# Optimization experiments

Measured on AMD Instinct MI355X. Metric: run time of the kernel, lower is better.

Reference implementation:

```python
import jax, jax.numpy as jnp
import numpy as np

B, D, E, H, TOP_K = 8192, 1024, 16, 1024, 8
LOSS_COEF = 0.01
NOISE_EPS = 0.01
INV_SQRT2 = 0.7071067811865476


def _normal_cdf(z):
    return 0.5 * (1.0 + jax.lax.erf(z * INV_SQRT2))


def _cv_squared(v):
    v = v.astype(jnp.float32)
    return jnp.var(v, ddof=1) / (jnp.mean(v) ** 2 + 1e-10)


def setup_inputs() -> dict:
    key = jax.random.key(0)
    k1, k2, k3, k4, k5, k6 = jax.random.split(key, 6)
    return {
        "x": jax.random.normal(k1, (B, D), dtype=jnp.float32),
        "w_gate": jax.random.normal(k2, (D, E), dtype=jnp.float32) * 0.02,
        "w_noise": jax.random.normal(k3, (D, E), dtype=jnp.float32) * 0.02,
        "expert_w": jax.random.normal(k4, (E, D, H), dtype=jnp.float32) * (1.0 / np.sqrt(D)),
        "expert_b": jax.random.normal(k5, (E, H), dtype=jnp.float32) * 0.01,
        "noise": jax.random.normal(k6, (B, E), dtype=jnp.float32),
    }


def reference(x, w_gate, w_noise, expert_w, expert_b, noise):
    # ---- noisy top-k gating (training=True) ----
    clean_logits = x @ w_gate                                   # [B, E]
    raw_noise_stddev = x @ w_noise                              # [B, E]
    noise_stddev = jax.nn.softplus(raw_noise_stddev) + NOISE_EPS
    noisy_logits = clean_logits + noise * noise_stddev          # [B, E]
    probs = jax.nn.softmax(noisy_logits, axis=1)                # [B, E]

    m = min(TOP_K + 1, E)
    top_logits, top_indices = jax.lax.top_k(probs, m)           # [B, m]
    top_k_logits = top_logits[:, :TOP_K]
    top_k_indices = top_indices[:, :TOP_K]
    top_k_gates = top_k_logits / (jnp.sum(top_k_logits, axis=1, keepdims=True) + 1e-6)

    rows = jnp.arange(B)[:, None]
    gates = jnp.zeros_like(probs).at[rows, top_k_indices].set(top_k_gates)  # [B, E]

    # ---- prob-in-top-k load (top_k < num_experts, training) ----
    # faithful to source: thresholds come from softmaxed top values,
    # compared against pre-softmax noisy/clean logits (as in original code)
    threshold_if_in = top_logits[:, TOP_K][:, None]             # [B, 1]
    threshold_if_out = top_logits[:, TOP_K - 1][:, None]        # [B, 1]
    is_in = noisy_logits > threshold_if_in
    prob_if_in = _normal_cdf((clean_logits - threshold_if_in) / noise_stddev)
    prob_if_out = _normal_cdf((clean_logits - threshold_if_out) / noise_stddev)
    load = jnp.where(is_in, prob_if_in, prob_if_out).sum(axis=0)  # [E]

    importance = gates.sum(axis=0)                              # [E]
    loss = LOSS_COEF * (_cv_squared(importance) + _cv_squared(load))

    # ---- experts: per-expert linear, gate-weighted sum over experts ----
    # y[b,h] = sum_e gates[b,e] * (x[b,:] @ W[e] + b[e])[h]
    y = jnp.einsum('bd,edh,be->bh', x, expert_w, gates) + gates @ expert_b
    return y, loss
```

## Files before the change

### kernel.cpp

```cpp
#include <hip/hip_runtime.h>
#include <cstdint>

#define B_SZ 8192
#define D_SZ 1024
#define E_SZ 16
#define H_SZ 1024
#define MAXTILES 544

using short8 = __attribute__((ext_vector_type(8))) short;
using f32x4  = __attribute__((ext_vector_type(4))) float;

__device__ __forceinline__ unsigned short f2bf(float f) {
  union { float f; unsigned int u; } v; v.f = f;
  unsigned int u = v.u;
  return (unsigned short)((u + 0x7fffu + ((u >> 16) & 1u)) >> 16);
}
__device__ __forceinline__ float bf2f(unsigned short h) {
  union { unsigned int u; float f; } v; v.u = ((unsigned int)h) << 16; return v.f;
}

__device__ __forceinline__ void async_ld16(void* lds, const void* g) {
  __builtin_amdgcn_global_load_lds(
      reinterpret_cast<const unsigned int __attribute__((address_space(1)))*>(
          reinterpret_cast<uintptr_t>(g)),
      reinterpret_cast<unsigned int __attribute__((address_space(3)))*>(
          reinterpret_cast<uintptr_t>(lds)),
      16, 0, 0);
}

__global__ __launch_bounds__(256) void prep(
    const float* __restrict__ x, const float* __restrict__ wg,
    const float* __restrict__ wn, const float* __restrict__ ew,
    unsigned short* __restrict__ xb, unsigned short* __restrict__ wtb,
    float* __restrict__ cl, float* __restrict__ rn, float* __restrict__ stats) {
  __shared__ __align__(16) float psm[2 * 32 * 132];
  const int bx = blockIdx.x;
  const int tid = threadIdx.x;

  if (bx < 256) {
    float* sx  = psm;
    float* swT = psm + 32 * 132;
    const int lane = tid & 63;
    const int wave = tid >> 6;
    const int row  = lane & 31;
    const int half = lane >> 5;
    const int rowbase = bx * 32;
    float acc[8] = {0.f, 0.f, 0.f, 0.f, 0.f, 0.f, 0.f, 0.f};

    const int srow = tid >> 3;
    const int sd   = (tid & 7) * 16;
    const int wd   = tid >> 1;
    const int wc   = (tid & 1) * 16;
    const float* wsrc = (wc == 0) ? wg : wn;

    for (int ch = 0; ch < 8; ++ch) {
      __syncthreads();
      #pragma unroll
      for (int k = 0; k < 4; ++k) {
        const float4 v = *(const float4*)(
            x + (size_t)(rowbase + srow) * D_SZ + ch * 128 + sd + k * 4);
        *(float4*)&sx[srow * 132 + sd + k * 4] = v;
      }
      {
        const float* wp = wsrc + (size_t)(ch * 128 + wd) * 16;
        float wv[16];
        #pragma unroll
        for (int k = 0; k < 4; ++k)
          *(float4*)&wv[k * 4] = *(const float4*)(wp + k * 4);
        #pragma unroll
        for (int j = 0; j < 16; ++j) swT[(wc + j) * 132 + wd] = wv[j];
      }
      __syncthreads();
      #pragma unroll 4
      for (int dg = 0; dg < 16; ++dg) {
        const int d = half * 64 + dg * 4;
        const f32x4 xv = *(const f32x4*)&sx[row * 132 + d];
        #pragma unroll
        for (int c = 0; c < 8; ++c) {
          const f32x4 wv = *(const f32x4*)&swT[(wave * 8 + c) * 132 + d];
          acc[c] = fmaf(xv[0], wv[0], acc[c]);
          acc[c] = fmaf(xv[1], wv[1], acc[c]);
          acc[c] = fmaf(xv[2], wv[2], acc[c]);
          acc[c] = fmaf(xv[3], wv[3], acc[c]);
        }
      }
    }
    #pragma unroll
    for (int c = 0; c < 8; ++c) acc[c] += __shfl_down(acc[c], 32);
    if (lane < 32) {
      const int cg = wave * 8;
      float* dst = (cg < 16) ? (cl + (size_t)(rowbase + row) * 16 + cg)
                             : (rn + (size_t)(rowbase + row) * 16 + (cg - 16));
      *(float4*)dst = *(const float4*)&acc[0];
      *(float4*)(dst + 4) = *(const float4*)&acc[4];
    }
  } else if (bx < 4352) {
    const int b = bx - 256;
    const size_t i = (size_t)b * 256 + tid;
    const float4 v0 = ((const float4*)x)[2 * i];
    const float4 v1 = ((const float4*)x)[2 * i + 1];
    unsigned short r[8] = {f2bf(v0.x), f2bf(v0.y), f2bf(v0.z), f2bf(v0.w),
                           f2bf(v1.x), f2bf(v1.y), f2bf(v1.z), f2bf(v1.w)};
    ((short8*)xb)[i] = *(const short8*)r;
    if (b == 0 && tid < 48) stats[tid] = 0.0f;
  } else {
    float (*t)[65] = (float(*)[65])psm;
    const int b = bx - 4352;
    const int e  = b >> 8;
    const int d0 = ((b >> 4) & 15) * 64;
    const int h0 = (b & 15) * 64;
    const float* We = ew + (size_t)e * D_SZ * H_SZ;
    unsigned short* Wte = wtb + (size_t)e * D_SZ * H_SZ;
    #pragma unroll
    for (int i = 0; i < 4; ++i) {
      const int idx = i * 256 + tid;
      const int r = idx >> 4, co = (idx & 15) * 4;
      *(float4*)&t[r][co] =
          *(const float4*)(We + (size_t)(d0 + r) * H_SZ + h0 + co);
    }
    __syncthreads();
    #pragma unroll
    for (int i = 0; i < 2; ++i) {
      const int idx = i * 256 + tid;
      const int r = idx >> 3, c8 = (idx & 7) * 8;
      unsigned short v[8];
      #pragma unroll
      for (int j = 0; j < 8; ++j) v[j] = f2bf(t[c8 + j][r]);
      *(short8*)(Wte + (size_t)(h0 + r) * D_SZ + d0 + c8) = *(const short8*)v;
    }
  }
}

__global__ __launch_bounds__(64) void gating_post(
    const float* __restrict__ clg, const float* __restrict__ rng,
    const float* __restrict__ noise, float* __restrict__ gates,
    float* __restrict__ stats, int* __restrict__ rowidx, int* __restrict__ rowmap) {
  int* gcount = (int*)(stats + 32);
  __shared__ int lcnt[16];
  __shared__ int lbase[16];
  const int row = blockIdx.x * 64 + threadIdx.x;
  if (threadIdx.x < 16) lcnt[threadIdx.x] = 0;
  float cl[16], sd[16], nl[16], p[16];
  #pragma unroll
  for (int e = 0; e < 16; ++e) {
    cl[e] = clg[(size_t)row * 16 + e];
    const float r = rng[(size_t)row * 16 + e];
    sd[e] = fmaxf(r, 0.0f) + log1pf(expf(-fabsf(r))) + 0.01f;
    nl[e] = cl[e] + noise[(size_t)row * 16 + e] * sd[e];
  }
  float mx = nl[0];
  #pragma unroll
  for (int e = 1; e < 16; ++e) mx = fmaxf(mx, nl[e]);
  float sum = 0.0f;
  #pragma unroll
  for (int e = 0; e < 16; ++e) { p[e] = expf(nl[e] - mx); sum += p[e]; }
  const float inv = 1.0f / sum;
  #pragma unroll
  for (int e = 0; e < 16; ++e) p[e] *= inv;
  float tmp[16];
  #pragma unroll
  for (int e = 0; e < 16; ++e) tmp[e] = p[e];
  float tv[9]; int ti[9];
  for (int k = 0; k < 9; ++k) {
    float bv = tmp[0]; int bj = 0;
    #pragma unroll
    for (int j = 1; j < 16; ++j) if (tmp[j] > bv) { bv = tmp[j]; bj = j; }
    tv[k] = bv; ti[k] = bj; tmp[bj] = -1.0f;
  }
  float s8 = 0.0f;
  #pragma unroll
  for (int k = 0; k < 8; ++k) s8 += tv[k];
  const float denom = s8 + 1e-6f;
  float g[16];
  #pragma unroll
  for (int e = 0; e < 16; ++e) g[e] = 0.0f;
  for (int k = 0; k < 8; ++k) g[ti[k]] = tv[k] / denom;
  const float thr_in = tv[8], thr_out = tv[7];
  float lc[16];
  #pragma unroll
  for (int e = 0; e < 16; ++e) {
    const float t = (nl[e] > thr_in) ? thr_in : thr_out;
    lc[e] = 0.5f * (1.0f + erff(((cl[e] - t) / sd[e]) * 0.70710678118654752f));
  }
  #pragma unroll
  for (int e = 0; e < 16; ++e) gates[(size_t)row * 16 + e] = g[e];
  __syncthreads();
  int myslot[8];
  #pragma unroll
  for (int k = 0; k < 8; ++k) myslot[k] = atomicAdd(&lcnt[ti[k]], 1);
  __syncthreads();
  if (threadIdx.x < 16) lbase[threadIdx.x] = atomicAdd(&gcount[threadIdx.x], lcnt[threadIdx.x]);
  __syncthreads();
  #pragma unroll
  for (int k = 0; k < 8; ++k) {
    const int e = ti[k];
    const int slot = lbase[e] + myslot[k];
    rowidx[e * B_SZ + slot] = row;
    rowmap[row * 8 + k] = (e << 13) | slot;
  }
  #pragma unroll
  for (int e = 0; e < 16; ++e) {
    float vi = g[e], vl = lc[e];
    for (int o = 32; o > 0; o >>= 1) { vi += __shfl_down(vi, o); vl += __shfl_down(vl, o); }
    if (threadIdx.x == 0) {
      atomicAdd(&stats[e], vi);
      atomicAdd(&stats[16 + e], vl);
    }
  }
}

__global__ __launch_bounds__(512, 4) void moe_gemm(
    const unsigned short* __restrict__ Xb,
    const unsigned short* __restrict__ Wt,
    const float* __restrict__ gates,
    const float* __restrict__ ebias,
    const float* __restrict__ stats,
    const int* __restrict__ rowidx,
    unsigned short* __restrict__ partial) {
  __shared__ __align__(16) char smem[49152 + 512 + 512];
  int*   sRI = (int*)(smem + 49152);
  float* sGG = (float*)(smem + 49664);

  const int orig = (int)blockIdx.x;
  const int logical = (orig & 7) * 272 + (orig >> 3);
  const int tileY = logical >> 2;
  const int col  = logical & 3;

  const int* gcount = (const int*)(stats + 32);
  int my_e = -1, tile = 0, tstart = 0, acc_t = 0;
  #pragma unroll
  for (int ee = 0; ee < 16; ++ee) {
    const int nt_e = (gcount[ee] + 127) >> 7;
    if (my_e < 0 && tileY < acc_t + nt_e) {
      my_e = ee; tile = tileY - acc_t; tstart = acc_t;
    }
    acc_t += nt_e;
  }
  if (my_e < 0) return;
  const int e = my_e;
  const int slot0 = tile << 7;
  const int cnt = gcount[e];
  const int col0 = col << 8;

  const int tid  = (int)threadIdx.x;
  const int lane = tid & 63;
  const int wave = tid >> 6;
  const int wm = wave >> 2, wn = wave & 3;
  const int ml = lane & 15;
  const int quad = lane >> 4;
  const int wb = tid & ~63;

  if (tid < 128) {
    const int slot = slot0 + tid;
    const int ok = slot < cnt;
    const int row = ok ? rowidx[e * B_SZ + slot] : 0;
    sRI[tid] = row;
    sGG[tid] = ok ? gates[(size_t)row * 16 + e] : 0.0f;
  }
  __syncthreads();

  const int sr = tid >> 2;
  const int sc = (tid & 3) ^ (sr & 3);
  const unsigned short* const We = Wt + (size_t)e * D_SZ * H_SZ;
  const unsigned short* a_srcp = Xb + (size_t)sRI[sr] * D_SZ + sc * 8;
  const unsigned short* b_src0 = We + (size_t)(col0 + sr) * D_SZ + sc * 8;
  const unsigned short* b_src1 = b_src0 + 128 * D_SZ;

#define STG(kt) do {                                                        \
    const int o_ = ((kt) & 1);                                              \
    async_ld16(smem + o_ * 8192 + (wb << 4), a_srcp + (kt) * 32);           \
    async_ld16(smem + 16384 + o_ * 16384 + (wb << 4), b_src0 + (kt) * 32);  \
    async_ld16(smem + 16384 + o_ * 16384 + 8192 + (wb << 4),                \
               b_src1 + (kt) * 32);                                         \
  } while (0)

  STG(0);
  __syncthreads();

  f32x4 acc[4][4] = {};
  float ebv[4];
  #pragma unroll
  for (int j = 0; j < 4; ++j)
    ebv[j] = ebias[(size_t)e * H_SZ + col0 + wn * 64 + j * 16 + ml];

  #pragma unroll 2
  for (int kt = 0; kt < 32; ++kt) {
    if (kt + 1 < 32) STG(kt + 1);
    const unsigned short* sA = (const unsigned short*)(smem + (kt & 1) * 8192);
    const unsigned short* sB =
        (const unsigned short*)(smem + 16384 + (kt & 1) * 16384);
    short8 af[4], bfr[4];
    #pragma unroll
    for (int i = 0; i < 4; ++i) {
      const int m = wm * 64 + i * 16 + ml;
      af[i] = *(const short8*)(sA + m * 32 + (quad ^ (m & 3)) * 8);
    }
    #pragma unroll
    for (int j = 0; j < 4; ++j) {
      const int n = wn * 64 + j * 16 + ml;
      bfr[j] = *(const short8*)(sB + n * 32 + (quad ^ (n & 3)) * 8);
    }
    __builtin_amdgcn_s_setprio(1);
    #pragma unroll
    for (int i = 0; i < 4; ++i)
      #pragma unroll
      for (int j = 0; j < 4; ++j)
        acc[i][j] = __builtin_amdgcn_mfma_f32_16x16x32_bf16(
            af[i], bfr[j], acc[i][j], 0, 0, 0);
    __builtin_amdgcn_s_setprio(0);
    __syncthreads();
  }
#undef STG

  unsigned short* sOut = (unsigned short*)smem;
  const size_t prow0 = (size_t)((tstart << 7) + slot0);
  #pragma unroll
  for (int h = 0; h < 2; ++h) {
    if (wm == h) {
      #pragma unroll
      for (int i = 0; i < 4; ++i) {
        const int lr = i * 16 + quad * 4;
        #pragma unroll
        for (int r = 0; r < 4; ++r) {
          const float gv = sGG[h * 64 + lr + r];
          #pragma unroll
          for (int j = 0; j < 4; ++j) {
            const int cc = wn * 64 + j * 16 + ml;
            sOut[(lr + r) * 264 + cc] = f2bf(gv * (acc[i][j][r] + ebv[j]));
          }
        }
      }
    }
    __syncthreads();
    #pragma unroll
    for (int it = 0; it < 4; ++it) {
      const int s = it * 512 + tid;
      const int rr = s >> 5;
      const int c8 = (s & 31) * 8;
      const short8 v = *(const short8*)(sOut + rr * 264 + c8);
      __builtin_nontemporal_store(
          v, (short8*)(partial + (prow0 + h * 64 + rr) * H_SZ + col0 + c8));
    }
    __syncthreads();
  }
}

__global__ __launch_bounds__(256) void reduce_k(
    const unsigned short* __restrict__ partial, const int* __restrict__ rowmap,
    const float* __restrict__ stats, float* __restrict__ y) {
  const int row0 = blockIdx.x * 4;
  const int tid = threadIdx.x;
  const int* gcount = (const int*)(stats + 32);
  __shared__ int sp[4][8];
  if (tid < 32) {
    const int r = tid >> 3, k = tid & 7;
    const int v = rowmap[(row0 + r) * 8 + k];
    const int e = v >> 13, slot = v & 8191;
    int t = 0;
    #pragma unroll
    for (int ee = 0; ee < 16; ++ee) t += (ee < e) ? ((gcount[ee] + 127) >> 7) : 0;
    sp[r][k] = (t << 7) + slot;
  }
  __syncthreads();
  const int r = tid >> 6;
  const int c0 = (tid & 63) * 16;
  float a[16];
  #pragma unroll
  for (int j = 0; j < 16; ++j) a[j] = 0.f;
  #pragma unroll
  for (int k = 0; k < 8; ++k) {
    const unsigned short* pp = partial + (size_t)sp[r][k] * H_SZ + c0;
    const short8 p0 = *(const short8*)pp;
    const short8 p1 = *(const short8*)(pp + 8);
    #pragma unroll
    for (int j = 0; j < 8; ++j) {
      a[j]     += bf2f((unsigned short)p0[j]);
      a[j + 8] += bf2f((unsigned short)p1[j]);
    }
  }
  float* yp = y + (size_t)(row0 + r) * H_SZ + c0;
  #pragma unroll
  for (int q = 0; q < 4; ++q) {
    float4 o = {a[q * 4], a[q * 4 + 1], a[q * 4 + 2], a[q * 4 + 3]};
    *(float4*)(yp + q * 4) = o;
  }

  if (blockIdx.x == 0 && tid == 0) {
    double si = 0.0, sl = 0.0;
    for (int e = 0; e < 16; ++e) { si += stats[e]; sl += stats[16 + e]; }
    const double mi = si / 16.0, mld = sl / 16.0;
    double vi = 0.0, vl = 0.0;
    for (int e = 0; e < 16; ++e) {
      const double di = stats[e] - mi;       vi += di * di;
      const double dl = stats[16 + e] - mld; vl += dl * dl;
    }
    vi /= 15.0; vl /= 15.0;
    const double loss = 0.01 * (vi / (mi * mi + 1e-10) + vl / (mld * mld + 1e-10));
    y[(size_t)B_SZ * H_SZ] = (float)loss;
  }
}

extern "C" void kernel_launch(void* const* d_in, const int* in_sizes, int n_in,
                              void* d_out, int out_size, void* d_ws, size_t ws_size,
                              hipStream_t stream) {
  (void)in_sizes; (void)n_in; (void)out_size; (void)ws_size;
  const float* x    = (const float*)d_in[0];
  const float* wg   = (const float*)d_in[1];
  const float* wnoi = (const float*)d_in[2];
  const float* ew   = (const float*)d_in[3];
  const float* eb   = (const float*)d_in[4];
  const float* nz   = (const float*)d_in[5];
  float* y = (float*)d_out;

  char* ws = (char*)d_ws;
  const size_t MB = 1024 * 1024;
  unsigned short* xb     = (unsigned short*)(ws);
  unsigned short* wtb    = (unsigned short*)(ws + 16 * MB);
  float* cl              = (float*)(ws + 48 * MB);
  float* rn              = (float*)(ws + 48 * MB + 512 * 1024);
  float* gates           = (float*)(ws + 49 * MB);
  int*   rowidx          = (int*)  (ws + 49 * MB + 512 * 1024);
  int*   rowmap          = (int*)  (ws + 50 * MB);
  float* stats           = (float*)(ws + 50 * MB + 512 * 1024);
  unsigned short* partial= (unsigned short*)(ws + 52 * MB);

  hipLaunchKernelGGL(prep,        dim3(8448),          dim3(256), 0, stream,
                     x, wg, wnoi, ew, xb, wtb, cl, rn, stats);
  hipLaunchKernelGGL(gating_post, dim3(128),           dim3(64),  0, stream,
                     cl, rn, nz, gates, stats, rowidx, rowmap);
  hipLaunchKernelGGL(moe_gemm,    dim3(4 * MAXTILES),  dim3(512), 0, stream,
                     xb, wtb, gates, eb, stats, rowidx, partial);
  hipLaunchKernelGGL(reduce_k,    dim3(2048),          dim3(256), 0, stream,
                     partial, rowmap, stats, y);
}
```

Measured before the change: 392.7 us.

## Enlarge MoE GEMM M-tile to 256 rows and load B fragments directly to registers

The grouped expert GEMM tile grows from 128x256 to 256x256 with a K-step of 64, halving the number of tiles and doubling reuse of each weight fragment. B operands now go straight from global memory into registers, double-buffered, rather than through LDS, and only A is staged asynchronously into LDS with an 8-way XOR swizzle. Occupancy drops to 2 blocks per CU, padding waste per expert grows, and the partial-output stores are no longer nontemporal. The reduce kernel's tile-offset math is updated to match.

Result: slower. 462.3 us (+17.7%).

```diff
diff --git a/kernel.cpp b/kernel.cpp
--- a/kernel.cpp
+++ b/kernel.cpp
@@ -5,7 +5,7 @@
 #define D_SZ 1024
 #define E_SZ 16
 #define H_SZ 1024
-#define MAXTILES 544
+#define MAXTILES 272
 
 using short8 = __attribute__((ext_vector_type(8))) short;
 using f32x4  = __attribute__((ext_vector_type(4))) float;
@@ -209,7 +209,7 @@
   }
 }
 
-__global__ __launch_bounds__(512, 4) void moe_gemm(
+__global__ __launch_bounds__(512, 2) void moe_gemm(
     const unsigned short* __restrict__ Xb,
     const unsigned short* __restrict__ Wt,
     const float* __restrict__ gates,
@@ -217,12 +217,12 @@
     const float* __restrict__ stats,
     const int* __restrict__ rowidx,
     unsigned short* __restrict__ partial) {
-  __shared__ __align__(16) char smem[49152 + 512 + 512];
-  int*   sRI = (int*)(smem + 49152);
-  float* sGG = (float*)(smem + 49664);
+  __shared__ __align__(16) char smem[69632];
+  int*   sRI = (int*)(smem + 67584);
+  float* sGG = (float*)(smem + 68608);
 
   const int orig = (int)blockIdx.x;
-  const int logical = (orig & 7) * 272 + (orig >> 3);
+  const int logical = (orig & 7) * (4 * MAXTILES / 8) + (orig >> 3);
   const int tileY = logical >> 2;
   const int col  = logical & 3;
 
@@ -230,7 +230,7 @@
   int my_e = -1, tile = 0, tstart = 0, acc_t = 0;
   #pragma unroll
   for (int ee = 0; ee < 16; ++ee) {
-    const int nt_e = (gcount[ee] + 127) >> 7;
+    const int nt_e = (gcount[ee] + 255) >> 8;
     if (my_e < 0 && tileY < acc_t + nt_e) {
       my_e = ee; tile = tileY - acc_t; tstart = acc_t;
     }
@@ -238,7 +238,7 @@
   }
   if (my_e < 0) return;
   const int e = my_e;
-  const int slot0 = tile << 7;
+  const int slot0 = tile << 8;
   const int cnt = gcount[e];
   const int col0 = col << 8;
 
@@ -250,7 +250,7 @@
   const int quad = lane >> 4;
   const int wb = tid & ~63;
 
-  if (tid < 128) {
+  if (tid < 256) {
     const int slot = slot0 + tid;
     const int ok = slot < cnt;
     const int row = ok ? rowidx[e * B_SZ + slot] : 0;
@@ -259,70 +259,86 @@
   }
   __syncthreads();
 
-  const int sr = tid >> 2;
-  const int sc = (tid & 3) ^ (sr & 3);
+  const int gc = (tid & 7) ^ ((tid >> 3) & 7);
+  const int rl = tid >> 3;
   const unsigned short* const We = Wt + (size_t)e * D_SZ * H_SZ;
-  const unsigned short* a_srcp = Xb + (size_t)sRI[sr] * D_SZ + sc * 8;
-  const unsigned short* b_src0 = We + (size_t)(col0 + sr) * D_SZ + sc * 8;
-  const unsigned short* b_src1 = b_src0 + 128 * D_SZ;
-
-#define STG(kt) do {                                                        \
-    const int o_ = ((kt) & 1);                                              \
-    async_ld16(smem + o_ * 8192 + (wb << 4), a_srcp + (kt) * 32);           \
-    async_ld16(smem + 16384 + o_ * 16384 + (wb << 4), b_src0 + (kt) * 32);  \
-    async_ld16(smem + 16384 + o_ * 16384 + 8192 + (wb << 4),                \
-               b_src1 + (kt) * 32);                                         \
+  const unsigned short* a_src0 = Xb + (size_t)sRI[rl]       * D_SZ + gc * 8;
+  const unsigned short* a_src1 = Xb + (size_t)sRI[64 + rl]  * D_SZ + gc * 8;
+  const unsigned short* a_src2 = Xb + (size_t)sRI[128 + rl] * D_SZ + gc * 8;
+  const unsigned short* a_src3 = Xb + (size_t)sRI[192 + rl] * D_SZ + gc * 8;
+
+  const unsigned short* bp[4];
+  #pragma unroll
+  for (int j = 0; j < 4; ++j)
+    bp[j] = We + (size_t)(col0 + wn * 64 + j * 16 + ml) * D_SZ + quad * 8;
+
+#define STG_A(kt) do {                                                        \
+    async_ld16(smem + (((kt) & 1) * 32768) + ((0 * 512 + wb) << 4),           \
+               a_src0 + (kt) * 64);                                           \
+    async_ld16(smem + (((kt) & 1) * 32768) + ((1 * 512 + wb) << 4),           \
+               a_src1 + (kt) * 64);                                           \
+    async_ld16(smem + (((kt) & 1) * 32768) + ((2 * 512 + wb) << 4),           \
+               a_src2 + (kt) * 64);                                           \
+    async_ld16(smem + (((kt) & 1) * 32768) + ((3 * 512 + wb) << 4),           \
+               a_src3 + (kt) * 64);                                           \
   } while (0)
 
-  STG(0);
-  __syncthreads();
-
-  f32x4 acc[4][4] = {};
+  short8 bf[2][4][2];
+#define LD_B(kt) do {                                                         \
+    _Pragma("unroll") for (int j = 0; j < 4; ++j)                             \
+      _Pragma("unroll") for (int kk = 0; kk < 2; ++kk)                        \
+        bf[(kt) & 1][j][kk] =                                                 \
+            *(const short8*)(bp[j] + (kt) * 64 + kk * 32);                    \
+  } while (0)
+
+  STG_A(0); LD_B(0);
+  f32x4 acc[8][4] = {};
+
+  #pragma unroll
+  for (int kt = 0; kt < 16; ++kt) {
+    asm volatile("s_waitcnt vmcnt(0)" ::: "memory");
+    __builtin_amdgcn_s_barrier();
+    if (kt + 1 < 16) { STG_A(kt + 1); LD_B(kt + 1); }
+    const unsigned short* sAb =
+        (const unsigned short*)(smem + ((kt & 1) ? 32768 : 0));
+    __builtin_amdgcn_s_setprio(1);
+    #pragma unroll
+    for (int i = 0; i < 8; ++i) {
+      const int m = wm * 128 + i * 16 + ml;
+      const short8 a0 =
+          *(const short8*)(sAb + (size_t)(m * 8 + (quad ^ (m & 7))) * 8);
+      const short8 a1 =
+          *(const short8*)(sAb + (size_t)(m * 8 + ((4 + quad) ^ (m & 7))) * 8);
+      #pragma unroll
+      for (int j = 0; j < 4; ++j) {
+        acc[i][j] = __builtin_amdgcn_mfma_f32_16x16x32_bf16(
+            a0, bf[kt & 1][j][0], acc[i][j], 0, 0, 0);
+        acc[i][j] = __builtin_amdgcn_mfma_f32_16x16x32_bf16(
+            a1, bf[kt & 1][j][1], acc[i][j], 0, 0, 0);
+      }
+    }
+    __builtin_amdgcn_s_setprio(0);
+    asm volatile("s_waitcnt lgkmcnt(0)" ::: "memory");
+  }
+#undef LD_B
+#undef STG_A
+
+  __syncthreads();
   float ebv[4];
   #pragma unroll
   for (int j = 0; j < 4; ++j)
     ebv[j] = ebias[(size_t)e * H_SZ + col0 + wn * 64 + j * 16 + ml];
-
-  #pragma unroll 2
-  for (int kt = 0; kt < 32; ++kt) {
-    if (kt + 1 < 32) STG(kt + 1);
-    const unsigned short* sA = (const unsigned short*)(smem + (kt & 1) * 8192);
-    const unsigned short* sB =
-        (const unsigned short*)(smem + 16384 + (kt & 1) * 16384);
-    short8 af[4], bfr[4];
-    #pragma unroll
-    for (int i = 0; i < 4; ++i) {
-      const int m = wm * 64 + i * 16 + ml;
-      af[i] = *(const short8*)(sA + m * 32 + (quad ^ (m & 3)) * 8);
-    }
-    #pragma unroll
-    for (int j = 0; j < 4; ++j) {
-      const int n = wn * 64 + j * 16 + ml;
-      bfr[j] = *(const short8*)(sB + n * 32 + (quad ^ (n & 3)) * 8);
-    }
-    __builtin_amdgcn_s_setprio(1);
-    #pragma unroll
-    for (int i = 0; i < 4; ++i)
+  unsigned short* sOut = (unsigned short*)smem;
+  const size_t prow0 = (size_t)((tstart << 8) + slot0);
+  #pragma unroll
+  for (int half = 0; half < 2; ++half) {
+    if (wm == half) {
       #pragma unroll
-      for (int j = 0; j < 4; ++j)
-        acc[i][j] = __builtin_amdgcn_mfma_f32_16x16x32_bf16(
-            af[i], bfr[j], acc[i][j], 0, 0, 0);
-    __builtin_amdgcn_s_setprio(0);
-    __syncthreads();
-  }
-#undef STG
-
-  unsigned short* sOut = (unsigned short*)smem;
-  const size_t prow0 = (size_t)((tstart << 7) + slot0);
-  #pragma unroll
-  for (int h = 0; h < 2; ++h) {
-    if (wm == h) {
-      #pragma unroll
-      for (int i = 0; i < 4; ++i) {
+      for (int i = 0; i < 8; ++i) {
         const int lr = i * 16 + quad * 4;
         #pragma unroll
         for (int r = 0; r < 4; ++r) {
-          const float gv = sGG[h * 64 + lr + r];
+          const float gv = sGG[half * 128 + lr + r];
           #pragma unroll
           for (int j = 0; j < 4; ++j) {
             const int cc = wn * 64 + j * 16 + ml;
@@ -333,13 +349,12 @@
     }
     __syncthreads();
     #pragma unroll
-    for (int it = 0; it < 4; ++it) {
+    for (int it = 0; it < 8; ++it) {
       const int s = it * 512 + tid;
       const int rr = s >> 5;
       const int c8 = (s & 31) * 8;
       const short8 v = *(const short8*)(sOut + rr * 264 + c8);
-      __builtin_nontemporal_store(
-          v, (short8*)(partial + (prow0 + h * 64 + rr) * H_SZ + col0 + c8));
+      *(short8*)(partial + (prow0 + half * 128 + rr) * H_SZ + col0 + c8) = v;
     }
     __syncthreads();
   }
@@ -358,8 +373,8 @@
     const int e = v >> 13, slot = v & 8191;
     int t = 0;
     #pragma unroll
-    for (int ee = 0; ee < 16; ++ee) t += (ee < e) ? ((gcount[ee] + 127) >> 7) : 0;
-    sp[r][k] = (t << 7) + slot;
+    for (int ee = 0; ee < 16; ++ee) t += (ee < e) ? ((gcount[ee] + 255) >> 8) : 0;
+    sp[r][k] = (t << 8) + slot;
   }
   __syncthreads();
   const int r = tid >> 6;
```

## Widen MoE GEMM tiles to 128x512 with 1024-thread blocks

Applied to the files above, without the earlier changes.

The grouped expert GEMM now uses 1024-thread blocks that each compute a 128-row by 512-column tile instead of 128x256 with 512 threads. The gathered X tile is loaded once per 512 columns instead of once per 256, which halves redundant A-tile reads and the grid size. The LDS swizzle changes from XOR to a rotation, tile-to-expert mapping covers two column halves per expert, and the epilogue writes in four column passes using regular stores instead of nontemporal ones. Occupancy drops to one large block per CU with about 81KB of LDS, which may leave less room to hide latency.

Result: slower. 405.4 us (+3.2%).

```diff
diff --git a/kernel.cpp b/kernel.cpp
--- a/kernel.cpp
+++ b/kernel.cpp
@@ -209,7 +209,7 @@
   }
 }
 
-__global__ __launch_bounds__(512, 4) void moe_gemm(
+__global__ __launch_bounds__(1024, 1) void moe_gemm(
     const unsigned short* __restrict__ Xb,
     const unsigned short* __restrict__ Wt,
     const float* __restrict__ gates,
@@ -217,38 +217,39 @@
     const float* __restrict__ stats,
     const int* __restrict__ rowidx,
     unsigned short* __restrict__ partial) {
-  __shared__ __align__(16) char smem[49152 + 512 + 512];
-  int*   sRI = (int*)(smem + 49152);
-  float* sGG = (float*)(smem + 49664);
+  __shared__ __align__(16) char smem[82944];
+  int*   sRI = (int*)(smem + 81920);
+  float* sGG = (float*)(smem + 82432);
 
   const int orig = (int)blockIdx.x;
-  const int logical = (orig & 7) * 272 + (orig >> 3);
-  const int tileY = logical >> 2;
-  const int col  = logical & 3;
+  const int logical = (orig & 7) * 136 + (orig >> 3);
 
   const int* gcount = (const int*)(stats + 32);
-  int my_e = -1, tile = 0, tstart = 0, acc_t = 0;
+  int my_e = -1, tile = 0, cb = 0, tstart = 0, acc_t = 0, t128 = 0;
   #pragma unroll
   for (int ee = 0; ee < 16; ++ee) {
     const int nt_e = (gcount[ee] + 127) >> 7;
-    if (my_e < 0 && tileY < acc_t + nt_e) {
-      my_e = ee; tile = tileY - acc_t; tstart = acc_t;
-    }
-    acc_t += nt_e;
+    if (my_e < 0 && logical < acc_t + 2 * nt_e) {
+      const int sub = logical - acc_t;
+      cb = (sub >= nt_e) ? 1 : 0;
+      tile = sub - (cb ? nt_e : 0);
+      my_e = ee; tstart = t128;
+    }
+    acc_t += 2 * nt_e;
+    t128 += nt_e;
   }
   if (my_e < 0) return;
   const int e = my_e;
   const int slot0 = tile << 7;
   const int cnt = gcount[e];
-  const int col0 = col << 8;
+  const int col0 = cb * 512;
 
   const int tid  = (int)threadIdx.x;
   const int lane = tid & 63;
   const int wave = tid >> 6;
-  const int wm = wave >> 2, wn = wave & 3;
+  const int wm = wave >> 3, wn = wave & 7;
   const int ml = lane & 15;
   const int quad = lane >> 4;
-  const int wb = tid & ~63;
 
   if (tid < 128) {
     const int slot = slot0 + tid;
@@ -259,46 +260,51 @@
   }
   __syncthreads();
 
-  const int sr = tid >> 2;
-  const int sc = (tid & 3) ^ (sr & 3);
   const unsigned short* const We = Wt + (size_t)e * D_SZ * H_SZ;
-  const unsigned short* a_srcp = Xb + (size_t)sRI[sr] * D_SZ + sc * 8;
-  const unsigned short* b_src0 = We + (size_t)(col0 + sr) * D_SZ + sc * 8;
-  const unsigned short* b_src1 = b_src0 + 128 * D_SZ;
-
-#define STG(kt) do {                                                        \
-    const int o_ = ((kt) & 1);                                              \
-    async_ld16(smem + o_ * 8192 + (wb << 4), a_srcp + (kt) * 32);           \
-    async_ld16(smem + 16384 + o_ * 16384 + (wb << 4), b_src0 + (kt) * 32);  \
-    async_ld16(smem + 16384 + o_ * 16384 + 8192 + (wb << 4),                \
-               b_src1 + (kt) * 32);                                         \
+  const unsigned short* a_src = 0;
+  if (tid < 512) {
+    const int r = tid >> 2;
+    const int g = ((tid & 3) - ((tid >> 3) & 3)) & 3;
+    a_src = Xb + (size_t)sRI[r] * D_SZ + g * 8;
+  }
+  const int r0 = tid >> 2;
+  const int g0 = ((tid & 3) - ((tid >> 3) & 3)) & 3;
+  const int r1 = (1024 + tid) >> 2;
+  const int g1 = (((1024 + tid) & 3) - (((1024 + tid) >> 3) & 3)) & 3;
+  const unsigned short* b_src0 = We + (size_t)(col0 + r0) * D_SZ + g0 * 8;
+  const unsigned short* b_src1 = We + (size_t)(col0 + r1) * D_SZ + g1 * 8;
+
+#define STG(kt) do {                                                          \
+    if (tid < 512)                                                            \
+      async_ld16(smem + (((kt) & 1) * 8192) + tid * 16, a_src + (kt) * 32);   \
+    async_ld16(smem + 16384 + (((kt) & 1) * 32768) + tid * 16,                \
+               b_src0 + (kt) * 32);                                           \
+    async_ld16(smem + 16384 + (((kt) & 1) * 32768) + 16384 + tid * 16,        \
+               b_src1 + (kt) * 32);                                           \
   } while (0)
 
   STG(0);
   __syncthreads();
 
   f32x4 acc[4][4] = {};
-  float ebv[4];
-  #pragma unroll
-  for (int j = 0; j < 4; ++j)
-    ebv[j] = ebias[(size_t)e * H_SZ + col0 + wn * 64 + j * 16 + ml];
 
   #pragma unroll 2
   for (int kt = 0; kt < 32; ++kt) {
     if (kt + 1 < 32) STG(kt + 1);
-    const unsigned short* sA = (const unsigned short*)(smem + (kt & 1) * 8192);
+    const unsigned short* sA =
+        (const unsigned short*)(smem + (kt & 1) * 8192);
     const unsigned short* sB =
-        (const unsigned short*)(smem + 16384 + (kt & 1) * 16384);
+        (const unsigned short*)(smem + 16384 + (kt & 1) * 32768);
     short8 af[4], bfr[4];
     #pragma unroll
     for (int i = 0; i < 4; ++i) {
       const int m = wm * 64 + i * 16 + ml;
-      af[i] = *(const short8*)(sA + m * 32 + (quad ^ (m & 3)) * 8);
+      af[i] = *(const short8*)(sA + m * 32 + ((quad + (m >> 1)) & 3) * 8);
     }
     #pragma unroll
     for (int j = 0; j < 4; ++j) {
       const int n = wn * 64 + j * 16 + ml;
-      bfr[j] = *(const short8*)(sB + n * 32 + (quad ^ (n & 3)) * 8);
+      bfr[j] = *(const short8*)(sB + n * 32 + ((quad + (n >> 1)) & 3) * 8);
     }
     __builtin_amdgcn_s_setprio(1);
     #pragma unroll
@@ -312,34 +318,37 @@
   }
 #undef STG
 
+  float ebv[4];
+  #pragma unroll
+  for (int j = 0; j < 4; ++j)
+    ebv[j] = ebias[(size_t)e * H_SZ + col0 + wn * 64 + j * 16 + ml];
   unsigned short* sOut = (unsigned short*)smem;
   const size_t prow0 = (size_t)((tstart << 7) + slot0);
   #pragma unroll
-  for (int h = 0; h < 2; ++h) {
-    if (wm == h) {
+  for (int p = 0; p < 4; ++p) {
+    if ((wn >> 1) == p) {
       #pragma unroll
       for (int i = 0; i < 4; ++i) {
-        const int lr = i * 16 + quad * 4;
+        const int lr = wm * 64 + i * 16 + quad * 4;
         #pragma unroll
         for (int r = 0; r < 4; ++r) {
-          const float gv = sGG[h * 64 + lr + r];
+          const float gv = sGG[lr + r];
           #pragma unroll
           for (int j = 0; j < 4; ++j) {
-            const int cc = wn * 64 + j * 16 + ml;
-            sOut[(lr + r) * 264 + cc] = f2bf(gv * (acc[i][j][r] + ebv[j]));
+            const int cc = (wn & 1) * 64 + j * 16 + ml;
+            sOut[(lr + r) * 136 + cc] = f2bf(gv * (acc[i][j][r] + ebv[j]));
           }
         }
       }
     }
     __syncthreads();
     #pragma unroll
-    for (int it = 0; it < 4; ++it) {
-      const int s = it * 512 + tid;
-      const int rr = s >> 5;
-      const int c8 = (s & 31) * 8;
-      const short8 v = *(const short8*)(sOut + rr * 264 + c8);
-      __builtin_nontemporal_store(
-          v, (short8*)(partial + (prow0 + h * 64 + rr) * H_SZ + col0 + c8));
+    for (int it = 0; it < 2; ++it) {
+      const int s = it * 1024 + tid;
+      const int rr = s >> 4;
+      const int c8 = (s & 15) * 8;
+      const short8 v = *(const short8*)(sOut + rr * 136 + c8);
+      *(short8*)(partial + (prow0 + rr) * H_SZ + col0 + p * 128 + c8) = v;
     }
     __syncthreads();
   }
@@ -424,12 +433,12 @@
   float* stats           = (float*)(ws + 50 * MB + 512 * 1024);
   unsigned short* partial= (unsigned short*)(ws + 52 * MB);
 
-  hipLaunchKernelGGL(prep,        dim3(8448),          dim3(256), 0, stream,
+  hipLaunchKernelGGL(prep,        dim3(8448),          dim3(256),  0, stream,
                      x, wg, wnoi, ew, xb, wtb, cl, rn, stats);
-  hipLaunchKernelGGL(gating_post, dim3(128),           dim3(64),  0, stream,
+  hipLaunchKernelGGL(gating_post, dim3(128),           dim3(64),   0, stream,
                      cl, rn, nz, gates, stats, rowidx, rowmap);
-  hipLaunchKernelGGL(moe_gemm,    dim3(4 * MAXTILES),  dim3(512), 0, stream,
+  hipLaunchKernelGGL(moe_gemm,    dim3(2 * MAXTILES),  dim3(1024), 0, stream,
                      xb, wtb, gates, eb, stats, rowidx, partial);
-  hipLaunchKernelGGL(reduce_k,    dim3(2048),          dim3(256), 0, stream,
+  hipLaunchKernelGGL(reduce_k,    dim3(2048),          dim3(256),  0, stream,
                      partial, rowmap, stats, y);
 }
```
